# Performance work log

Measured on AMD Instinct MI355X. Metric: run time of the kernel, lower is better.

Reference implementation:

```python
import jax, jax.numpy as jnp
import numpy as np

SQRT3 = 3.0 ** 0.5


def setup_inputs() -> dict:
    key = jax.random.key(0)
    k1, k2 = jax.random.split(key)
    N, M, D = 8192, 4096, 64
    X = jax.random.normal(k1, (N, D), dtype=jnp.float32)
    Z = jax.random.normal(k2, (M, D), dtype=jnp.float32)
    sigma = jnp.asarray(1.0, dtype=jnp.float32)
    lengthscale = jnp.asarray(2.0, dtype=jnp.float32)
    return {"X": X, "Z": Z, "sigma": sigma, "lengthscale": lengthscale}


def reference(X, Z, sigma, lengthscale):
    # Pairwise squared distances via GEMM expansion (avoids [N,M,D] diff tensor).
    x2 = jnp.sum(X * X, axis=-1)[:, None]            # [N,1]
    z2 = jnp.sum(Z * Z, axis=-1)[None, :]            # [1,M]
    sq = x2 + z2 - 2.0 * jnp.einsum('nd,md->nm', X, Z)  # [N,M]
    dist = jnp.sqrt(jnp.maximum(sq, 1e-12))
    val = SQRT3 * dist / lengthscale
    return (sigma ** 2) * (1.0 + val) * jnp.exp(-val)  # [N,M] Matern-3/2 Gram
```

## Files before the change

### kernel.cpp

```cpp
#include <hip/hip_runtime.h>
#include <math.h>

#define SQRT3F 1.7320508075688772f

typedef _Float16 half8 __attribute__((ext_vector_type(8)));
typedef _Float16 half4 __attribute__((ext_vector_type(4)));
typedef float    f32x4 __attribute__((ext_vector_type(4)));

__global__ __launch_bounds__(512, 4)
void matern_mfma_kernel(const float* __restrict__ X,
                        const float* __restrict__ Z,
                        const float* __restrict__ sigma,
                        const float* __restrict__ lengthscale,
                        float* __restrict__ out,
                        int M) {
    __shared__ _Float16 Ah[128][72];
    __shared__ _Float16 Al[128][72];
    __shared__ _Float16 Bh[128][72];
    __shared__ _Float16 Bl[128][72];
    __shared__ float    x2s[128];
    __shared__ float    z2s[128];

    const int t  = threadIdx.x;
    const int n0 = blockIdx.x * 128;
    const int m0 = blockIdx.y * 128;

    {
        float4 vx[4], vz[4];
        #pragma unroll
        for (int i = 0; i < 4; ++i) {
            const int f = t + 512 * i;
            vx[i] = *(const float4*)(X + (size_t)(m0 + (f >> 4)) * 64 + (f & 15) * 4);
        }
        #pragma unroll
        for (int i = 0; i < 4; ++i) {
            const int f = t + 512 * i;
            vz[i] = *(const float4*)(Z + (size_t)(n0 + (f >> 4)) * 64 + (f & 15) * 4);
        }
        #pragma unroll
        for (int i = 0; i < 4; ++i) {
            const int f   = t + 512 * i;
            const int row = f >> 4;
            const int c4  = f & 15;
            float4 v = vx[i];
            _Float16 hx = (_Float16)v.x, hy = (_Float16)v.y, hz = (_Float16)v.z, hw = (_Float16)v.w;
            half4 hv = { hx, hy, hz, hw };
            half4 lv = { (_Float16)(v.x - (float)hx), (_Float16)(v.y - (float)hy),
                         (_Float16)(v.z - (float)hz), (_Float16)(v.w - (float)hw) };
            *(half4*)&Ah[row][c4 * 4] = hv;
            *(half4*)&Al[row][c4 * 4] = lv;
            float ssq = v.x * v.x + v.y * v.y + v.z * v.z + v.w * v.w;
            ssq += __shfl_xor(ssq, 1, 16);
            ssq += __shfl_xor(ssq, 2, 16);
            ssq += __shfl_xor(ssq, 4, 16);
            ssq += __shfl_xor(ssq, 8, 16);
            if ((t & 15) == 0) x2s[row] = ssq;
        }
        #pragma unroll
        for (int i = 0; i < 4; ++i) {
            const int f   = t + 512 * i;
            const int row = f >> 4;
            const int c4  = f & 15;
            float4 v = vz[i];
            _Float16 hx = (_Float16)v.x, hy = (_Float16)v.y, hz = (_Float16)v.z, hw = (_Float16)v.w;
            half4 hv = { hx, hy, hz, hw };
            half4 lv = { (_Float16)(v.x - (float)hx), (_Float16)(v.y - (float)hy),
                         (_Float16)(v.z - (float)hz), (_Float16)(v.w - (float)hw) };
            *(half4*)&Bh[row][c4 * 4] = hv;
            *(half4*)&Bl[row][c4 * 4] = lv;
            float ssq = v.x * v.x + v.y * v.y + v.z * v.z + v.w * v.w;
            ssq += __shfl_xor(ssq, 1, 16);
            ssq += __shfl_xor(ssq, 2, 16);
            ssq += __shfl_xor(ssq, 4, 16);
            ssq += __shfl_xor(ssq, 8, 16);
            if ((t & 15) == 0) z2s[row] = ssq;
        }
    }
    __syncthreads();

    const int lane = t & 63;
    const int w    = t >> 6;
    const int wr   = w >> 2;
    const int wc   = w & 3;
    const int lm   = lane & 15;
    const int q    = lane >> 4;

    f32x4 acc[4][2];
    #pragma unroll
    for (int a = 0; a < 4; ++a)
        #pragma unroll
        for (int b = 0; b < 2; ++b)
            acc[a][b] = (f32x4){0.f, 0.f, 0.f, 0.f};

    #pragma unroll
    for (int kc = 0; kc < 2; ++kc) {
        const int k = kc * 32 + q * 8;
        half8 ah[4], al[4], bh[2], bl[2];
        #pragma unroll
        for (int mt = 0; mt < 4; ++mt) {
            const int row = wr * 64 + mt * 16 + lm;
            ah[mt] = *(const half8*)&Ah[row][k];
            al[mt] = *(const half8*)&Al[row][k];
        }
        #pragma unroll
        for (int nt = 0; nt < 2; ++nt) {
            const int row = wc * 32 + nt * 16 + lm;
            bh[nt] = *(const half8*)&Bh[row][k];
            bl[nt] = *(const half8*)&Bl[row][k];
        }
        #pragma unroll
        for (int mt = 0; mt < 4; ++mt)
            #pragma unroll
            for (int nt = 0; nt < 2; ++nt) {
                acc[mt][nt] = __builtin_amdgcn_mfma_f32_16x16x32_f16(ah[mt], bh[nt], acc[mt][nt], 0, 0, 0);
                acc[mt][nt] = __builtin_amdgcn_mfma_f32_16x16x32_f16(ah[mt], bl[nt], acc[mt][nt], 0, 0, 0);
                acc[mt][nt] = __builtin_amdgcn_mfma_f32_16x16x32_f16(al[mt], bh[nt], acc[mt][nt], 0, 0, 0);
            }
    }

    const float s   = sigma[0];
    const float l   = lengthscale[0];
    const float fac = SQRT3F / l;
    const float s2  = s * s;

    #pragma unroll
    for (int mt = 0; mt < 4; ++mt) {
        const int row0 = wr * 64 + mt * 16 + q * 4;
        float xr[4];
        #pragma unroll
        for (int r = 0; r < 4; ++r) xr[r] = x2s[row0 + r];
        #pragma unroll
        for (int nt = 0; nt < 2; ++nt) {
            const int col = wc * 32 + nt * 16 + lm;
            const float zc = z2s[col];
            #pragma unroll
            for (int r = 0; r < 4; ++r) {
                float sq  = xr[r] + zc - 2.0f * acc[mt][nt][r];
                float d   = __builtin_amdgcn_sqrtf(fmaxf(sq, 1e-12f));
                float val = fac * d;
                out[(size_t)(m0 + row0 + r) * (size_t)M + n0 + col] =
                    s2 * (1.0f + val) * __expf(-val);
            }
        }
    }
}

extern "C" void kernel_launch(void* const* d_in, const int* in_sizes, int n_in,
                              void* d_out, int out_size, void* d_ws, size_t ws_size,
                              hipStream_t stream) {
    (void)n_in; (void)out_size; (void)d_ws; (void)ws_size;
    const float* X   = (const float*)d_in[0];
    const float* Z   = (const float*)d_in[1];
    const float* sig = (const float*)d_in[2];
    const float* len = (const float*)d_in[3];
    float* out = (float*)d_out;

    const int D = 64;
    const int N = in_sizes[0] / D;
    const int M = in_sizes[1] / D;

    dim3 grid(M / 128, N / 128);
    matern_mfma_kernel<<<grid, 512, 0, stream>>>(X, Z, sig, len, out, M);
}
```

Measured before the change: 152.9 us.

## Split fp16 hi/lo conversion into a prep kernel and read fragments from global

Adds a prep kernel that converts X and Z once into fp16 high/low halves plus row norms in workspace. The main kernel then drops shared memory and __syncthreads and loads MFMA fragments straight from global memory. Its tile shrinks to 128x64 with 256 threads, and output uses nontemporal stores. This removes the per-block redundant conversion and LDS staging, at the cost of an extra launch and uncoalesced-ish global fragment loads served from cache.

```diff
diff --git a/kernel.cpp b/kernel.cpp
--- a/kernel.cpp
+++ b/kernel.cpp
@@ -7,81 +7,50 @@
 typedef _Float16 half4 __attribute__((ext_vector_type(4)));
 typedef float    f32x4 __attribute__((ext_vector_type(4)));
 
-__global__ __launch_bounds__(512, 4)
-void matern_mfma_kernel(const float* __restrict__ X,
-                        const float* __restrict__ Z,
-                        const float* __restrict__ sigma,
-                        const float* __restrict__ lengthscale,
-                        float* __restrict__ out,
-                        int M) {
-    __shared__ _Float16 Ah[128][72];
-    __shared__ _Float16 Al[128][72];
-    __shared__ _Float16 Bh[128][72];
-    __shared__ _Float16 Bl[128][72];
-    __shared__ float    x2s[128];
-    __shared__ float    z2s[128];
 
-    const int t  = threadIdx.x;
-    const int n0 = blockIdx.x * 128;
-    const int m0 = blockIdx.y * 128;
+__global__ __launch_bounds__(256)
+void matern_prep_kernel(const float* __restrict__ X, const float* __restrict__ Z,
+                        _Float16* __restrict__ Xh, _Float16* __restrict__ Xl,
+                        _Float16* __restrict__ Zh, _Float16* __restrict__ Zl,
+                        float* __restrict__ x2, float* __restrict__ z2,
+                        int N, int M) {
+    int f = blockIdx.x * 256 + threadIdx.x;
+    const int totX = N * 16;
+    const int tot  = (N + M) * 16;
+    if (f >= tot) return;
+    const float* src; _Float16 *dh, *dl; float* nrm;
+    if (f < totX) { src = X; dh = Xh; dl = Xl; nrm = x2; }
+    else          { f -= totX; src = Z; dh = Zh; dl = Zl; nrm = z2; }
 
-    {
-        float4 vx[4], vz[4];
-        #pragma unroll
-        for (int i = 0; i < 4; ++i) {
-            const int f = t + 512 * i;
-            vx[i] = *(const float4*)(X + (size_t)(m0 + (f >> 4)) * 64 + (f & 15) * 4);
-        }
-        #pragma unroll
-        for (int i = 0; i < 4; ++i) {
-            const int f = t + 512 * i;
-            vz[i] = *(const float4*)(Z + (size_t)(n0 + (f >> 4)) * 64 + (f & 15) * 4);
-        }
-        #pragma unroll
-        for (int i = 0; i < 4; ++i) {
-            const int f   = t + 512 * i;
-            const int row = f >> 4;
-            const int c4  = f & 15;
-            float4 v = vx[i];
-            _Float16 hx = (_Float16)v.x, hy = (_Float16)v.y, hz = (_Float16)v.z, hw = (_Float16)v.w;
-            half4 hv = { hx, hy, hz, hw };
-            half4 lv = { (_Float16)(v.x - (float)hx), (_Float16)(v.y - (float)hy),
-                         (_Float16)(v.z - (float)hz), (_Float16)(v.w - (float)hw) };
-            *(half4*)&Ah[row][c4 * 4] = hv;
-            *(half4*)&Al[row][c4 * 4] = lv;
-            float ssq = v.x * v.x + v.y * v.y + v.z * v.z + v.w * v.w;
-            ssq += __shfl_xor(ssq, 1, 16);
-            ssq += __shfl_xor(ssq, 2, 16);
-            ssq += __shfl_xor(ssq, 4, 16);
-            ssq += __shfl_xor(ssq, 8, 16);
-            if ((t & 15) == 0) x2s[row] = ssq;
-        }
-        #pragma unroll
-        for (int i = 0; i < 4; ++i) {
-            const int f   = t + 512 * i;
-            const int row = f >> 4;
-            const int c4  = f & 15;
-            float4 v = vz[i];
-            _Float16 hx = (_Float16)v.x, hy = (_Float16)v.y, hz = (_Float16)v.z, hw = (_Float16)v.w;
-            half4 hv = { hx, hy, hz, hw };
-            half4 lv = { (_Float16)(v.x - (float)hx), (_Float16)(v.y - (float)hy),
-                         (_Float16)(v.z - (float)hz), (_Float16)(v.w - (float)hw) };
-            *(half4*)&Bh[row][c4 * 4] = hv;
-            *(half4*)&Bl[row][c4 * 4] = lv;
-            float ssq = v.x * v.x + v.y * v.y + v.z * v.z + v.w * v.w;
-            ssq += __shfl_xor(ssq, 1, 16);
-            ssq += __shfl_xor(ssq, 2, 16);
-            ssq += __shfl_xor(ssq, 4, 16);
-            ssq += __shfl_xor(ssq, 8, 16);
-            if ((t & 15) == 0) z2s[row] = ssq;
-        }
-    }
-    __syncthreads();
+    float4 v = *(const float4*)(src + (size_t)f * 4);
+    _Float16 hx = (_Float16)v.x, hy = (_Float16)v.y, hz = (_Float16)v.z, hw = (_Float16)v.w;
+    half4 hv = { hx, hy, hz, hw };
+    half4 lv = { (_Float16)(v.x - (float)hx), (_Float16)(v.y - (float)hy),
+                 (_Float16)(v.z - (float)hz), (_Float16)(v.w - (float)hw) };
+    *(half4*)(dh + (size_t)f * 4) = hv;
+    *(half4*)(dl + (size_t)f * 4) = lv;
 
+    float ssq = v.x * v.x + v.y * v.y + v.z * v.z + v.w * v.w;
+    ssq += __shfl_xor(ssq, 1, 16);
+    ssq += __shfl_xor(ssq, 2, 16);
+    ssq += __shfl_xor(ssq, 4, 16);
+    ssq += __shfl_xor(ssq, 8, 16);
+    if ((threadIdx.x & 15) == 0) nrm[f >> 4] = ssq;
+}
+
+__global__ __launch_bounds__(256, 4)
+void matern_main_kernel(const _Float16* __restrict__ Xh, const _Float16* __restrict__ Xl,
+                        const _Float16* __restrict__ Zh, const _Float16* __restrict__ Zl,
+                        const float* __restrict__ x2, const float* __restrict__ z2,
+                        const float* __restrict__ sigma, const float* __restrict__ lengthscale,
+                        float* __restrict__ out, int M) {
+    const int t    = threadIdx.x;
     const int lane = t & 63;
     const int w    = t >> 6;
-    const int wr   = w >> 2;
-    const int wc   = w & 3;
+    const int wr   = w >> 1;
+    const int wc   = w & 1;
+    const int m0   = blockIdx.y * 128 + wr * 64;
+    const int n0   = blockIdx.x * 64  + wc * 32;
     const int lm   = lane & 15;
     const int q    = lane >> 4;
 
@@ -98,15 +67,15 @@
         half8 ah[4], al[4], bh[2], bl[2];
         #pragma unroll
         for (int mt = 0; mt < 4; ++mt) {
-            const int row = wr * 64 + mt * 16 + lm;
-            ah[mt] = *(const half8*)&Ah[row][k];
-            al[mt] = *(const half8*)&Al[row][k];
+            const int off = (m0 + mt * 16 + lm) * 64 + k;
+            ah[mt] = *(const half8*)(Xh + off);
+            al[mt] = *(const half8*)(Xl + off);
         }
         #pragma unroll
         for (int nt = 0; nt < 2; ++nt) {
-            const int row = wc * 32 + nt * 16 + lm;
-            bh[nt] = *(const half8*)&Bh[row][k];
-            bl[nt] = *(const half8*)&Bl[row][k];
+            const int off = (n0 + nt * 16 + lm) * 64 + k;
+            bh[nt] = *(const half8*)(Zh + off);
+            bl[nt] = *(const half8*)(Zl + off);
         }
         #pragma unroll
         for (int mt = 0; mt < 4; ++mt)
@@ -125,21 +94,20 @@
 
     #pragma unroll
     for (int mt = 0; mt < 4; ++mt) {
-        const int row0 = wr * 64 + mt * 16 + q * 4;
-        float xr[4];
-        #pragma unroll
-        for (int r = 0; r < 4; ++r) xr[r] = x2s[row0 + r];
+        const int row0 = m0 + mt * 16 + q * 4;
+        const f32x4 xr = *(const f32x4*)(x2 + row0);
         #pragma unroll
         for (int nt = 0; nt < 2; ++nt) {
-            const int col = wc * 32 + nt * 16 + lm;
-            const float zc = z2s[col];
+            const int col = n0 + nt * 16 + lm;
+            const float zc = z2[col];
+            float* op = out + (size_t)row0 * (size_t)M + col;
             #pragma unroll
             for (int r = 0; r < 4; ++r) {
                 float sq  = xr[r] + zc - 2.0f * acc[mt][nt][r];
                 float d   = __builtin_amdgcn_sqrtf(fmaxf(sq, 1e-12f));
                 float val = fac * d;
-                out[(size_t)(m0 + row0 + r) * (size_t)M + n0 + col] =
-                    s2 * (1.0f + val) * __expf(-val);
+                __builtin_nontemporal_store(s2 * (1.0f + val) * __expf(-val), op);
+                op += M;
             }
         }
     }
@@ -148,7 +116,7 @@
 extern "C" void kernel_launch(void* const* d_in, const int* in_sizes, int n_in,
                               void* d_out, int out_size, void* d_ws, size_t ws_size,
                               hipStream_t stream) {
-    (void)n_in; (void)out_size; (void)d_ws; (void)ws_size;
+    (void)n_in; (void)out_size; (void)ws_size;
     const float* X   = (const float*)d_in[0];
     const float* Z   = (const float*)d_in[1];
     const float* sig = (const float*)d_in[2];
@@ -159,6 +127,19 @@
     const int N = in_sizes[0] / D;
     const int M = in_sizes[1] / D;
 
-    dim3 grid(M / 128, N / 128);
-    matern_mfma_kernel<<<grid, 512, 0, stream>>>(X, Z, sig, len, out, M);
+    char* ws = (char*)d_ws;
+    size_t o = 0;
+    auto take = [&](size_t bytes) { char* p = ws + o; o += (bytes + 255) & ~(size_t)255; return p; };
+    _Float16* Xh = (_Float16*)take((size_t)N * D * sizeof(_Float16));
+    _Float16* Xl = (_Float16*)take((size_t)N * D * sizeof(_Float16));
+    _Float16* Zh = (_Float16*)take((size_t)M * D * sizeof(_Float16));
+    _Float16* Zl = (_Float16*)take((size_t)M * D * sizeof(_Float16));
+    float*    x2 = (float*)take((size_t)N * sizeof(float));
+    float*    z2 = (float*)take((size_t)M * sizeof(float));
+
+    const int tot = (N + M) * 16;
+    matern_prep_kernel<<<(tot + 255) / 256, 256, 0, stream>>>(X, Z, Xh, Xl, Zh, Zl, x2, z2, N, M);
+
+    dim3 grid(M / 64, N / 128);
+    matern_main_kernel<<<grid, 256, 0, stream>>>(Xh, Xl, Zh, Zl, x2, z2, sig, len, out, M);
 }
```

After: 184.0 us. +20.3%, slower.
